# Kernel tuning notes

Hardware: AMD Instinct MI355X
Metric: run time of the kernel (lower is better)

The kernel has to match this reference:

```python
import jax, jax.numpy as jnp
import numpy as np

N, E, D = 8192, 4096, 256
EDGE_DENSITY = 0.05  # ~410 nodes per hyperedge; guarantees no empty edge


def _layernorm(x, gamma, beta, eps=1e-5):
    mu = jnp.mean(x, axis=-1, keepdims=True)
    var = jnp.mean((x - mu) ** 2, axis=-1, keepdims=True)
    return (x - mu) * jax.lax.rsqrt(var + eps) * gamma + beta


def setup_inputs() -> dict:
    key = jax.random.key(0)
    k1, k2, k3 = jax.random.split(key, 3)
    node_embeddings = jax.random.normal(k1, (N, D), dtype=jnp.float32)
    # scale 1/sqrt(N) keeps two chained NxN matmuls per layer numerically sane
    target_martrix = jax.random.normal(k2, (N, N), dtype=jnp.float32) / np.float32(np.sqrt(N))
    hypergraph_matrix = (jax.random.uniform(k3, (N, E)) < EDGE_DENSITY).astype(jnp.float32)
    ln_gamma = jnp.ones((D,), jnp.float32)
    ln_beta = jnp.zeros((D,), jnp.float32)
    return {
        "node_embeddings": node_embeddings,
        "target_martrix": target_martrix,
        "hypergraph_matrix": hypergraph_matrix,
        "ln_gamma": ln_gamma,
        "ln_beta": ln_beta,
        "num_layers": 3,
    }


def reference(node_embeddings, target_martrix, hypergraph_matrix, ln_gamma, ln_beta, num_layers):
    # --- propagation: num_layers rounds of A @ x then A.T @ (.), residual + LN ---
    last = node_embeddings
    source = node_embeddings
    for _ in range(num_layers):
        t = target_martrix @ last            # [N, D]
        source = target_martrix.T @ t        # [N, D]  (pre-residual, pre-norm)
        last = _layernorm(source + node_embeddings, ln_gamma, ln_beta)
        # dropout p=0.35 is identity in eval mode
    # --- hyperedge masked-mean + global max (the torch per-edge python loop) ---
    # NOTE: torch loop uses `source_embedding` of the LAST layer (pre-norm).
    Hb = (hypergraph_matrix > 0).astype(source.dtype)   # [N, E]
    sums = Hb.T @ source                                 # [E, D] segment sums
    counts = jnp.sum(Hb, axis=0)[:, None]                # [E, 1] (all > 0 by construction)
    means = sums / counts                                # per-edge masked mean
    return jnp.max(means, axis=0)                        # [D]
```

## Files before the change

### kernel.cpp

```cpp
#include <hip/hip_runtime.h>


typedef __bf16 bf16;
typedef __bf16 bf16x8 __attribute__((ext_vector_type(8)));
typedef float f32x4 __attribute__((ext_vector_type(4)));

__device__ __forceinline__ void gld_lds16(const bf16* g, bf16* l) {
  __builtin_amdgcn_global_load_lds(
      (const __attribute__((address_space(1))) unsigned int*)g,
      (__attribute__((address_space(3))) unsigned int*)l, 16, 0, 0);
}

template <int BN>
__global__ __launch_bounds__(256) void gemm_bt(const bf16* __restrict__ A,
                                               const bf16* __restrict__ B,
                                               float* __restrict__ P,
                                               int N, int K, int Ks) {
  constexpr int BM = 256, BK = 64;
  constexpr int WM = 128, WN = BN / 2;
  constexpr int TM = WM / 16, TN = WN / 16;
  constexpr int QA = BM / 32, QB = BN / 32;

  __shared__ __align__(16) bf16 As[2][BM * BK];
  __shared__ __align__(16) bf16 Bs[2][BN * BK];

  const int t = threadIdx.x, w = t >> 6, l = t & 63;
  const int srow = l >> 3;
  const int schunk = (l & 7) ^ srow;
  const int n0 = blockIdx.x * BN;
  const int kbase = blockIdx.z * Ks;

  const bf16* gA = A + (size_t)(w * 8 + srow) * K + kbase + schunk * 8;
  const bf16* gB = B + (size_t)(n0 + w * 8 + srow) * K + kbase + schunk * 8;

  auto stage = [&](int kk, int buf) {
    const size_t ko = (size_t)kk * BK;
#pragma unroll
    for (int q = 0; q < QA; ++q)
      gld_lds16(gA + (size_t)(q * 32) * K + ko,
                &As[buf][(q * 32 + w * 8) * BK]);
#pragma unroll
    for (int q = 0; q < QB; ++q)
      gld_lds16(gB + (size_t)(q * 32) * K + ko,
                &Bs[buf][(q * 32 + w * 8) * BK]);
  };

  const int lm = l & 15, kq = l >> 4;
  const int wm = (w >> 1) * WM;
  const int wn = (w & 1) * WN;

  f32x4 acc[TM][TN] = {};
  const int nk = Ks / BK;

  stage(0, 0);
  __syncthreads();

  for (int kk = 0; kk < nk; ++kk) {
    const int buf = kk & 1;
    if (kk + 1 < nk) stage(kk + 1, buf ^ 1);
#pragma unroll
    for (int ks = 0; ks < 2; ++ks) {
      const int csw = ((ks * 4 + kq) ^ (lm & 7)) * 8;
      bf16x8 af[TM], bfr[TN];
#pragma unroll
      for (int i = 0; i < TM; ++i)
        af[i] = *(const bf16x8*)(&As[buf][(wm + i * 16 + lm) * BK + csw]);
#pragma unroll
      for (int j = 0; j < TN; ++j)
        bfr[j] = *(const bf16x8*)(&Bs[buf][(wn + j * 16 + lm) * BK + csw]);
#pragma unroll
      for (int i = 0; i < TM; ++i)
#pragma unroll
        for (int j = 0; j < TN; ++j)
          acc[i][j] = __builtin_amdgcn_mfma_f32_16x16x32_bf16(af[i], bfr[j],
                                                              acc[i][j], 0, 0, 0);
    }
    __syncthreads();
  }

  float* Pz = P + (size_t)blockIdx.z * BM * N;
#pragma unroll
  for (int i = 0; i < TM; ++i) {
    const int mrow = wm + i * 16 + kq * 4;
#pragma unroll
    for (int j = 0; j < TN; ++j) {
      const int col = n0 + wn + j * 16 + lm;
#pragma unroll
      for (int r = 0; r < 4; ++r)
        Pz[(size_t)(mrow + r) * N + col] = acc[i][j][r];
    }
  }
}

__global__ __launch_bounds__(256) void reduce4_bf16(const float* __restrict__ P,
                                                    bf16* __restrict__ out,
                                                    size_t MN) {
  const size_t i4 = ((size_t)blockIdx.x * 256 + threadIdx.x) * 4;
  if (i4 >= MN) return;
  f32x4 a = *(const f32x4*)(P + i4);
  f32x4 b = *(const f32x4*)(P + MN + i4);
  f32x4 c = *(const f32x4*)(P + 2 * MN + i4);
  f32x4 d = *(const f32x4*)(P + 3 * MN + i4);
  a = a + b + c + d;
  bf16 o[4] = {(bf16)a[0], (bf16)a[1], (bf16)a[2], (bf16)a[3]};
  *(int2*)(out + i4) = *(const int2*)o;
}

__global__ __launch_bounds__(256) void transpose_conv(
    const float* __restrict__ src, int R, int C, bf16* __restrict__ cpy,
    bf16* __restrict__ trb, float* __restrict__ trf) {
  __shared__ float tile[64][65];
  const int t = threadIdx.x;
  const int col = t & 63, rb4 = t >> 6;
  const int r0 = blockIdx.y * 64, c0 = blockIdx.x * 64;
#pragma unroll
  for (int rr = 0; rr < 64; rr += 4) {
    const int row = rr + rb4;
    const float v = src[(size_t)(r0 + row) * C + c0 + col];
    tile[row][col] = v;
    if (cpy) cpy[(size_t)(r0 + row) * C + c0 + col] = (bf16)v;
  }
  __syncthreads();
#pragma unroll
  for (int rr = 0; rr < 64; rr += 4) {
    const int row = rr + rb4;
    const float v = tile[col][row];
    const size_t di = (size_t)(c0 + row) * R + r0 + col;
    if (trb) trb[di] = (bf16)v;
    if (trf) trf[di] = v;
  }
}

__global__ __launch_bounds__(256) void ln_kernel(const float* __restrict__ P,
                                                 const float* __restrict__ x0t,
                                                 const float* __restrict__ gamma,
                                                 const float* __restrict__ beta,
                                                 bf16* __restrict__ Xt) {
  constexpr size_t MN = (size_t)256 * 8192;
  const int tx = threadIdx.x;
  const int ty = threadIdx.y;
  const int i = blockIdx.x * 32 + tx;
  float vbuf[32];
  float s = 0.f, s2 = 0.f;
#pragma unroll
  for (int dd = 0; dd < 32; ++dd) {
    const int d = ty * 32 + dd;
    const size_t idx = (size_t)d * 8192 + i;
    const float v = P[idx] + P[MN + idx] + P[2 * MN + idx] + P[3 * MN + idx] +
                    x0t[idx];
    vbuf[dd] = v;
    s += v;
    s2 += v * v;
  }
  __shared__ float S[8][32], Q[8][32];
  S[ty][tx] = s;
  Q[ty][tx] = s2;
  __syncthreads();
  __shared__ float MU[32], RS[32];
  if (ty == 0) {
    float a = 0.f, b = 0.f;
#pragma unroll
    for (int r = 0; r < 8; ++r) {
      a += S[r][tx];
      b += Q[r][tx];
    }
    const float mu = a * (1.0f / 256.0f);
    const float var = b * (1.0f / 256.0f) - mu * mu;
    MU[tx] = mu;
    RS[tx] = rsqrtf(var + 1e-5f);
  }
  __syncthreads();
  const float mu = MU[tx], rs = RS[tx];
#pragma unroll
  for (int dd = 0; dd < 32; ++dd) {
    const int d = ty * 32 + dd;
    const float y = (vbuf[dd] - mu) * rs * gamma[d] + beta[d];
    Xt[(size_t)d * 8192 + i] = (bf16)y;
  }
}

__global__ __launch_bounds__(256) void counts_kernel(const bf16* __restrict__ Htb,
                                                     float* __restrict__ invc) {
  const int e = blockIdx.x;
  const bf16* row = Htb + (size_t)e * 8192;
  float s = 0.f;
  for (int i = threadIdx.x; i < 8192; i += 256) s += (float)row[i];
  __shared__ float red[256];
  red[threadIdx.x] = s;
  __syncthreads();
  for (int k = 128; k > 0; k >>= 1) {
    if (threadIdx.x < k) red[threadIdx.x] += red[threadIdx.x + k];
    __syncthreads();
  }
  if (threadIdx.x == 0) invc[e] = 1.0f / red[0];
}

__global__ __launch_bounds__(256) void final_max(const float* __restrict__ P,
                                                 const float* __restrict__ invc,
                                                 float* __restrict__ out,
                                                 int S) {
  constexpr size_t MN = (size_t)256 * 4096;
  const int d = blockIdx.x;
  float m = -3.4e38f;
  for (int e = threadIdx.x; e < 4096; e += 256) {
    const size_t idx = (size_t)d * 4096 + e;
    float s = 0.f;
    for (int z = 0; z < S; ++z) s += P[z * MN + idx];
    m = fmaxf(m, s * invc[e]);
  }
  __shared__ float red[256];
  red[threadIdx.x] = m;
  __syncthreads();
  for (int k = 128; k > 0; k >>= 1) {
    if (threadIdx.x < k)
      red[threadIdx.x] = fmaxf(red[threadIdx.x], red[threadIdx.x + k]);
    __syncthreads();
  }
  if (threadIdx.x == 0) out[d] = red[0];
}

extern "C" void kernel_launch(void* const* d_in, const int* in_sizes, int n_in,
                              void* d_out, int out_size, void* d_ws,
                              size_t ws_size, hipStream_t stream) {
  const float* x0 = (const float*)d_in[0];
  const float* T = (const float*)d_in[1];
  const float* H = (const float*)d_in[2];
  const float* gamma = (const float*)d_in[3];
  const float* beta = (const float*)d_in[4];

  constexpr int Nn = 8192, E = 4096, D = 256, K = 8192;

  char* w = (char*)d_ws;
  size_t off = 0;
  auto carve = [&](size_t bytes) {
    char* p = w + off;
    off += (bytes + 255) & ~(size_t)255;
    return p;
  };
  bf16* Tb = (bf16*)carve((size_t)Nn * Nn * 2);
  bf16* Tt = (bf16*)carve((size_t)Nn * Nn * 2);
  bf16* Htb = (bf16*)carve((size_t)E * Nn * 2);
  float* x0t = (float*)carve((size_t)D * Nn * 4);
  bf16* Xt = (bf16*)carve((size_t)D * Nn * 2);
  bf16* tt = (bf16*)carve((size_t)D * Nn * 2);
  bf16* stb = (bf16*)carve((size_t)D * Nn * 2);
  float* invc = (float*)carve((size_t)E * 4);
  float* P = (float*)carve((size_t)4 * D * Nn * 4);

  if (off > ws_size) {
    hipMemsetAsync(d_out, 0, (size_t)out_size * 4, stream);
    return;
  }

  transpose_conv<<<dim3(128, 128), 256, 0, stream>>>(T, Nn, Nn, Tb, Tt, nullptr);
  transpose_conv<<<dim3(64, 128), 256, 0, stream>>>(H, Nn, E, nullptr, Htb, nullptr);
  transpose_conv<<<dim3(4, 128), 256, 0, stream>>>(x0, Nn, D, nullptr, Xt, x0t);
  counts_kernel<<<E, 256, 0, stream>>>(Htb, invc);

  const size_t MN = (size_t)D * Nn;
  for (int layer = 0; layer < 3; ++layer) {
    gemm_bt<128><<<dim3(64, 1, 4), 256, 0, stream>>>(Xt, Tb, P, Nn, K, K / 4);
    reduce4_bf16<<<(int)(MN / 1024), 256, 0, stream>>>(P, tt, MN);
    gemm_bt<128><<<dim3(64, 1, 4), 256, 0, stream>>>(tt, Tt, P, Nn, K, K / 4);
    if (layer < 2) {
      ln_kernel<<<dim3(256), dim3(32, 8), 0, stream>>>(P, x0t, gamma, beta, Xt);
    } else {
      reduce4_bf16<<<(int)(MN / 1024), 256, 0, stream>>>(P, stb, MN);
    }
  }

  gemm_bt<128><<<dim3(32, 1, 8), 256, 0, stream>>>(stb, Htb, P, E, K, K / 8);
  final_max<<<D, 256, 0, stream>>>(P, invc, (float*)d_out, 8);
}
```

Baseline: 1.091 ms.

## Enlarge GEMM tiles to 512 threads, prefetch two stages, raise split-K

The bf16 GEMM now runs 512-thread blocks over 256x256 tiles instead of 256x128. It issues two k-stages of async global-to-LDS loads up front and waits with explicit vmcnt counters and raw barriers, so a load stays in flight across each compute step. Split-K rises from 4 to 8 (16 for the hyperedge GEMM), and the reduce and layernorm kernels sum the extra partial slices. This aims to improve data reuse and latency hiding, but it doubles the fp32 partial-sum traffic and workspace and keeps the number of blocks at 256.

```diff
diff --git a/kernel.cpp b/kernel.cpp
--- a/kernel.cpp
+++ b/kernel.cpp
@@ -12,14 +12,13 @@
 }
 
 template <int BN>
-__global__ __launch_bounds__(256) void gemm_bt(const bf16* __restrict__ A,
+__global__ __launch_bounds__(512) void gemm_bt(const bf16* __restrict__ A,
                                                const bf16* __restrict__ B,
                                                float* __restrict__ P,
                                                int N, int K, int Ks) {
   constexpr int BM = 256, BK = 64;
-  constexpr int WM = 128, WN = BN / 2;
-  constexpr int TM = WM / 16, TN = WN / 16;
-  constexpr int QA = BM / 32, QB = BN / 32;
+  constexpr int TM = 8, TN = BN / 64;
+  constexpr int QA = BM / 64, QB = BN / 64;
 
   __shared__ __align__(16) bf16 As[2][BM * BK];
   __shared__ __align__(16) bf16 Bs[2][BN * BK];
@@ -37,37 +36,47 @@
     const size_t ko = (size_t)kk * BK;
 #pragma unroll
     for (int q = 0; q < QA; ++q)
-      gld_lds16(gA + (size_t)(q * 32) * K + ko,
-                &As[buf][(q * 32 + w * 8) * BK]);
+      gld_lds16(gA + (size_t)(q * 64) * K + ko,
+                &As[buf][(q * 64 + w * 8) * BK]);
 #pragma unroll
     for (int q = 0; q < QB; ++q)
-      gld_lds16(gB + (size_t)(q * 32) * K + ko,
-                &Bs[buf][(q * 32 + w * 8) * BK]);
+      gld_lds16(gB + (size_t)(q * 64) * K + ko,
+                &Bs[buf][(q * 64 + w * 8) * BK]);
   };
 
   const int lm = l & 15, kq = l >> 4;
-  const int wm = (w >> 1) * WM;
-  const int wn = (w & 1) * WN;
+  const int wm = (w >> 2) * 128;
+  const int wn = (w & 3) * (TN * 16);
 
   f32x4 acc[TM][TN] = {};
   const int nk = Ks / BK;
 
   stage(0, 0);
-  __syncthreads();
+  stage(1, 1);
 
   for (int kk = 0; kk < nk; ++kk) {
     const int buf = kk & 1;
-    if (kk + 1 < nk) stage(kk + 1, buf ^ 1);
+    if (kk + 1 < nk)
+      asm volatile("s_waitcnt vmcnt(8)" ::: "memory");
+    else
+      asm volatile("s_waitcnt vmcnt(0)" ::: "memory");
+    asm volatile("s_barrier" ::: "memory");
+
 #pragma unroll
     for (int ks = 0; ks < 2; ++ks) {
-      const int csw = ((ks * 4 + kq) ^ (lm & 7)) * 8;
       bf16x8 af[TM], bfr[TN];
 #pragma unroll
-      for (int i = 0; i < TM; ++i)
-        af[i] = *(const bf16x8*)(&As[buf][(wm + i * 16 + lm) * BK + csw]);
-#pragma unroll
-      for (int j = 0; j < TN; ++j)
-        bfr[j] = *(const bf16x8*)(&Bs[buf][(wn + j * 16 + lm) * BK + csw]);
+      for (int i = 0; i < TM; ++i) {
+        const int r = wm + i * 16 + lm;
+        const int c = ((ks * 4 + kq) ^ (r & 7)) * 8;
+        af[i] = *(const bf16x8*)(&As[buf][r * BK + c]);
+      }
+#pragma unroll
+      for (int j = 0; j < TN; ++j) {
+        const int r = wn + j * 16 + lm;
+        const int c = ((ks * 4 + kq) ^ (r & 7)) * 8;
+        bfr[j] = *(const bf16x8*)(&Bs[buf][r * BK + c]);
+      }
 #pragma unroll
       for (int i = 0; i < TM; ++i)
 #pragma unroll
@@ -75,7 +84,8 @@
           acc[i][j] = __builtin_amdgcn_mfma_f32_16x16x32_bf16(af[i], bfr[j],
                                                               acc[i][j], 0, 0, 0);
     }
-    __syncthreads();
+    asm volatile("s_barrier" ::: "memory");
+    if (kk + 2 < nk) stage(kk + 2, buf);
   }
 
   float* Pz = P + (size_t)blockIdx.z * BM * N;
@@ -92,16 +102,15 @@
   }
 }
 
-__global__ __launch_bounds__(256) void reduce4_bf16(const float* __restrict__ P,
+template <int S>
+__global__ __launch_bounds__(256) void reduceS_bf16(const float* __restrict__ P,
                                                     bf16* __restrict__ out,
                                                     size_t MN) {
   const size_t i4 = ((size_t)blockIdx.x * 256 + threadIdx.x) * 4;
   if (i4 >= MN) return;
   f32x4 a = *(const f32x4*)(P + i4);
-  f32x4 b = *(const f32x4*)(P + MN + i4);
-  f32x4 c = *(const f32x4*)(P + 2 * MN + i4);
-  f32x4 d = *(const f32x4*)(P + 3 * MN + i4);
-  a = a + b + c + d;
+#pragma unroll
+  for (int z = 1; z < S; ++z) a = a + *(const f32x4*)(P + (size_t)z * MN + i4);
   bf16 o[4] = {(bf16)a[0], (bf16)a[1], (bf16)a[2], (bf16)a[3]};
   *(int2*)(out + i4) = *(const int2*)o;
 }
@@ -146,8 +155,9 @@
   for (int dd = 0; dd < 32; ++dd) {
     const int d = ty * 32 + dd;
     const size_t idx = (size_t)d * 8192 + i;
-    const float v = P[idx] + P[MN + idx] + P[2 * MN + idx] + P[3 * MN + idx] +
-                    x0t[idx];
+    float v = x0t[idx];
+#pragma unroll
+    for (int z = 0; z < 8; ++z) v += P[(size_t)z * MN + idx];
     vbuf[dd] = v;
     s += v;
     s2 += v * v;
@@ -245,7 +255,7 @@
   bf16* tt = (bf16*)carve((size_t)D * Nn * 2);
   bf16* stb = (bf16*)carve((size_t)D * Nn * 2);
   float* invc = (float*)carve((size_t)E * 4);
-  float* P = (float*)carve((size_t)4 * D * Nn * 4);
+  float* P = (float*)carve((size_t)8 * D * Nn * 4);
 
   if (off > ws_size) {
     hipMemsetAsync(d_out, 0, (size_t)out_size * 4, stream);
@@ -259,16 +269,16 @@
 
   const size_t MN = (size_t)D * Nn;
   for (int layer = 0; layer < 3; ++layer) {
-    gemm_bt<128><<<dim3(64, 1, 4), 256, 0, stream>>>(Xt, Tb, P, Nn, K, K / 4);
-    reduce4_bf16<<<(int)(MN / 1024), 256, 0, stream>>>(P, tt, MN);
-    gemm_bt<128><<<dim3(64, 1, 4), 256, 0, stream>>>(tt, Tt, P, Nn, K, K / 4);
+    gemm_bt<256><<<dim3(32, 1, 8), 512, 0, stream>>>(Xt, Tb, P, Nn, K, K / 8);
+    reduceS_bf16<8><<<(int)(MN / 1024), 256, 0, stream>>>(P, tt, MN);
+    gemm_bt<256><<<dim3(32, 1, 8), 512, 0, stream>>>(tt, Tt, P, Nn, K, K / 8);
     if (layer < 2) {
       ln_kernel<<<dim3(256), dim3(32, 8), 0, stream>>>(P, x0t, gamma, beta, Xt);
     } else {
-      reduce4_bf16<<<(int)(MN / 1024), 256, 0, stream>>>(P, stb, MN);
-    }
-  }
-
-  gemm_bt<128><<<dim3(32, 1, 8), 256, 0, stream>>>(stb, Htb, P, E, K, K / 8);
-  final_max<<<D, 256, 0, stream>>>(P, invc, (float*)d_out, 8);
-}
+      reduceS_bf16<8><<<(int)(MN / 1024), 256, 0, stream>>>(P, stb, MN);
+    }
+  }
+
+  gemm_bt<256><<<dim3(16, 1, 16), 512, 0, stream>>>(stb, Htb, P, E, K, K / 16);
+  final_max<<<D, 256, 0, stream>>>(P, invc, (float*)d_out, 16);
+}
```

New measurement: 1.114 ms. +2.1%, slower.
